# Kernel optimization log

Hardware: AMD Instinct MI355X
Metric: run time of the kernel (lower is better)

Reference implementation:

```python
import jax, jax.numpy as jnp
import numpy as np

B, S, D = 32, 2048, 64

def setup_inputs() -> dict:
    key = jax.random.key(0)
    kq, kk, kv = jax.random.split(key, 3)
    return {
        "query": jax.random.normal(kq, (B, S, D), dtype=jnp.float32),
        "key": jax.random.normal(kk, (B, S, D), dtype=jnp.float32),
        "value": jax.random.normal(kv, (B, S, D), dtype=jnp.float32),
    }

def reference(query, key, value):
    # scores: [B, S, S] = Q @ K^T / sqrt(d_k)  (scale=True)
    d_k = key.shape[-1]
    scores = jnp.einsum("bqd,bkd->bqk", query, key) / jnp.sqrt(jnp.asarray(d_k, query.dtype))
    # exp + normalize over last dim == softmax (no mask, dropout in eval mode)
    attn = jax.nn.softmax(scores, axis=-1)
    # context: [B, S, D] = attn @ V
    context = jnp.einsum("bqk,bkd->bqd", attn, value)
    return context
```

## Files before the change

### kernel.cpp

```cpp
#include <hip/hip_runtime.h>
#include <hip/hip_bf16.h>

#define B_   32
#define S_   2048
#define D_   64
#define KVB  64
#define NT   (S_/KVB)
#define NW   8
#define QW   32
#define QB   (NW*QW)

typedef __attribute__((ext_vector_type(8)))  __bf16 bf16x8;
typedef __attribute__((ext_vector_type(4)))  __bf16 bf16x4;
typedef __attribute__((ext_vector_type(16))) float  f32x16;

__device__ __forceinline__ float fexp2(float x) {
#if __has_builtin(__builtin_amdgcn_exp2f)
    return __builtin_amdgcn_exp2f(x);
#else
    return exp2f(x);
#endif
}

__device__ __forceinline__ unsigned pk2(float a, float b) {
    unsigned r;
    asm("v_cvt_pk_bf16_f32 %0, %1, %2" : "=v"(r) : "v"(a), "v"(b));
    return r;
}

__device__ __forceinline__ void pl32swap(unsigned &a, unsigned &b) {
#if __has_builtin(__builtin_amdgcn_permlane32_swap)
    auto r = __builtin_amdgcn_permlane32_swap(a, b, false, false);
    a = (unsigned)r[0]; b = (unsigned)r[1];
#else
    unsigned pa = (unsigned)__shfl_xor((int)a, 32);
    unsigned pb = (unsigned)__shfl_xor((int)b, 32);
    bool hi = (threadIdx.x & 32) != 0;
    unsigned na = hi ? pb : a;
    unsigned nb = hi ? b  : pa;
    a = na; b = nb;
#endif
}

__device__ __forceinline__ f32x16 z16() {
    f32x16 z;
    #pragma unroll
    for (int i = 0; i < 16; ++i) z[i] = 0.f;
    return z;
}

struct PBpair { bf16x8 a, b; };

__device__ __forceinline__ PBpair pack2(const f32x16 ps) {
    unsigned y0 = pk2(ps[0],  ps[1]);
    unsigned y1 = pk2(ps[2],  ps[3]);
    unsigned y2 = pk2(ps[4],  ps[5]);
    unsigned y3 = pk2(ps[6],  ps[7]);
    pl32swap(y0, y2); pl32swap(y1, y3);
    unsigned z0 = pk2(ps[8],  ps[9]);
    unsigned z1 = pk2(ps[10], ps[11]);
    unsigned z2 = pk2(ps[12], ps[13]);
    unsigned z3 = pk2(ps[14], ps[15]);
    pl32swap(z0, z2); pl32swap(z1, z3);
    union { unsigned u[4]; bf16x8 v; } pa, pbu;
    pa.u[0]=y0;  pa.u[1]=y1;  pa.u[2]=y2;  pa.u[3]=y3;
    pbu.u[0]=z0; pbu.u[1]=z1; pbu.u[2]=z2; pbu.u[3]=z3;
    PBpair r; r.a = pa.v; r.b = pbu.v; return r;
}

__global__ __launch_bounds__(512, 2)
void attn_fwd(const float* __restrict__ Q, const float* __restrict__ K,
              const float* __restrict__ V, float* __restrict__ Out)
{
    __shared__ __align__(16) __bf16 Kt[3][KVB * D_];
    __shared__ __align__(16) __bf16 Vt[3][D_ * KVB];

    const int tid  = threadIdx.x;
    const int w    = tid >> 6;
    const int lane = tid & 63;
    const int l31  = lane & 31;
    const int hi   = lane >> 5;

    const int bid = blockIdx.x;
    const int swz = ((bid & 7) << 5) | (bid >> 3);
    const int b   = swz >> 3;
    const int q0  = (swz & 7) * QB;

    const float SCL = 0.18033688011112042f;
    const float* qp = Q + ((size_t)(b*S_ + q0 + w*QW + l31))*D_ + hi*8;
    bf16x8 qf[4];
    #pragma unroll
    for (int ks = 0; ks < 4; ++ks) {
        float4 f0 = *reinterpret_cast<const float4*>(qp + ks*16);
        float4 f1 = *reinterpret_cast<const float4*>(qp + ks*16 + 4);
        bf16x8 a;
        a[0]=(__bf16)(f0.x*SCL); a[1]=(__bf16)(f0.y*SCL);
        a[2]=(__bf16)(f0.z*SCL); a[3]=(__bf16)(f0.w*SCL);
        a[4]=(__bf16)(f1.x*SCL); a[5]=(__bf16)(f1.y*SCL);
        a[6]=(__bf16)(f1.z*SCL); a[7]=(__bf16)(f1.w*SCL);
        qf[ks]=a;
    }

    int offK[4], offV[4];
    #pragma unroll
    for (int i = 0; i < 4; ++i) {
        offK[i] = l31*128 + (((i*32) + hi*16) ^ ((l31 & 7) << 4));
        offV[i] = l31*128 + (((i*32) + hi*16) ^ (((l31 >> 1) & 7) << 4));
    }

    const float* kg = K + (size_t)b*S_*D_;
    const float* vg = V + (size_t)b*S_*D_;

    const int krow0 = tid >> 4;
    const int kcol  = (tid & 15) * 4;
    const int kwr0  = krow0*128 + ((kcol*2) ^ ((krow0 & 7) << 4));
    const int kwr1  = kwr0 + 32*128;

    const int kv0 = (tid >> 4) * 2;
    const int db  = (tid & 15) * 2;
    int vwr[4];
    #pragma unroll
    for (int j = 0; j < 4; ++j) {
        int d = db + (j >> 1)*32 + (j & 1);
        vwr[j] = d*128 + ((kv0*2) ^ (((d >> 1) & 7) << 4));
    }

#define STAGE_LOAD(T)                                                              \
    {   const float* kt_ = kg + (size_t)(T)*KVB*D_;                                \
        const float* vt_ = vg + (size_t)(T)*KVB*D_;                                \
        ka  = *reinterpret_cast<const float4*>(kt_ + krow0*64 + kcol);             \
        kb  = *reinterpret_cast<const float4*>(kt_ + (krow0+32)*64 + kcol);        \
        va0 = *reinterpret_cast<const float2*>(vt_ + kv0*64 + db);                 \
        vb0 = *reinterpret_cast<const float2*>(vt_ + (kv0+1)*64 + db);             \
        va1 = *reinterpret_cast<const float2*>(vt_ + kv0*64 + db + 32);            \
        vb1 = *reinterpret_cast<const float2*>(vt_ + (kv0+1)*64 + db + 32);        }

#define STAGE_WRITE(BUF)                                                           \
    {   char* kw = (char*)&Kt[(BUF)][0];                                           \
        char* vw = (char*)&Vt[(BUF)][0];                                           \
        bf16x4 h0 = {(__bf16)ka.x,(__bf16)ka.y,(__bf16)ka.z,(__bf16)ka.w};         \
        bf16x4 h1 = {(__bf16)kb.x,(__bf16)kb.y,(__bf16)kb.z,(__bf16)kb.w};         \
        *reinterpret_cast<bf16x4*>(kw + kwr0) = h0;                                \
        *reinterpret_cast<bf16x4*>(kw + kwr1) = h1;                                \
        *reinterpret_cast<unsigned*>(vw + vwr[0]) = pk2(va0.x, vb0.x);             \
        *reinterpret_cast<unsigned*>(vw + vwr[1]) = pk2(va0.y, vb0.y);             \
        *reinterpret_cast<unsigned*>(vw + vwr[2]) = pk2(va1.x, vb1.x);             \
        *reinterpret_cast<unsigned*>(vw + vwr[3]) = pk2(va1.y, vb1.y);             }

    float4 ka, kb; float2 va0, vb0, va1, vb1;

    STAGE_LOAD(0)
    STAGE_WRITE(0)
    __syncthreads();

    float l_ = 0.f;
    f32x16 o0 = z16(), o1 = z16();
    PBpair p01, p23;

    {
        STAGE_LOAD(1)
        const char* kbuf = (const char*)&Kt[0][0];
        f32x16 s0 = z16(), s1 = z16();
        __builtin_amdgcn_s_setprio(1);
        #pragma unroll
        for (int ks = 0; ks < 4; ++ks) {
            bf16x8 k0 = *reinterpret_cast<const bf16x8*>(kbuf + offK[ks]);
            bf16x8 k1 = *reinterpret_cast<const bf16x8*>(kbuf + offK[ks] + 4096);
            s0 = __builtin_amdgcn_mfma_f32_32x32x16_bf16(k0, qf[ks], s0, 0,0,0);
            s1 = __builtin_amdgcn_mfma_f32_32x32x16_bf16(k1, qf[ks], s1, 0,0,0);
        }
        __builtin_amdgcn_s_setprio(0);
        #pragma unroll
        for (int r = 0; r < 16; ++r) s0[r] = fexp2(s0[r]);
        #pragma unroll
        for (int r = 0; r < 16; ++r) s1[r] = fexp2(s1[r]);
        float tsm[16];
        #pragma unroll
        for (int i = 0; i < 16; ++i) tsm[i] = s0[i] + s1[i];
        #pragma unroll
        for (int st = 8; st > 0; st >>= 1)
            #pragma unroll
            for (int i = 0; i < st; ++i) tsm[i] += tsm[i+st];
        l_ += tsm[0] + __shfl_xor(tsm[0], 32);
        p01 = pack2(s0);
        p23 = pack2(s1);
        STAGE_WRITE(1)
        __syncthreads();
    }

    for (int t = 1; t < NT; ++t) {
        const int cur = t % 3;
        const int prv = (t-1) % 3;
        const int nxt = (t+1) % 3;
        const int tn  = (t+1 < NT) ? (t+1) : t;
        STAGE_LOAD(tn)

        const char* kbuf = (const char*)&Kt[cur][0];
        const char* vbuf = (const char*)&Vt[prv][0];

        f32x16 s0 = z16(), s1 = z16();
        __builtin_amdgcn_s_setprio(1);
        #pragma unroll
        for (int ks = 0; ks < 4; ++ks) {
            bf16x8 k0 = *reinterpret_cast<const bf16x8*>(kbuf + offK[ks]);
            bf16x8 k1 = *reinterpret_cast<const bf16x8*>(kbuf + offK[ks] + 4096);
            s0 = __builtin_amdgcn_mfma_f32_32x32x16_bf16(k0, qf[ks], s0, 0,0,0);
            s1 = __builtin_amdgcn_mfma_f32_32x32x16_bf16(k1, qf[ks], s1, 0,0,0);
        }
        #define PV_STEP(c, pbf)                                                        \
        {   bf16x8 v0 = *reinterpret_cast<const bf16x8*>(vbuf + offV[c]);              \
            bf16x8 v1 = *reinterpret_cast<const bf16x8*>(vbuf + offV[c] + 4096);       \
            o0 = __builtin_amdgcn_mfma_f32_32x32x16_bf16(v0, pbf, o0, 0,0,0);          \
            o1 = __builtin_amdgcn_mfma_f32_32x32x16_bf16(v1, pbf, o1, 0,0,0);          }
        PV_STEP(0, p01.a)
        PV_STEP(1, p01.b)
        PV_STEP(2, p23.a)
        PV_STEP(3, p23.b)
        __builtin_amdgcn_s_setprio(0);

        #pragma unroll
        for (int r = 0; r < 16; ++r) s0[r] = fexp2(s0[r]);
        #pragma unroll
        for (int r = 0; r < 16; ++r) s1[r] = fexp2(s1[r]);
        float tsm[16];
        #pragma unroll
        for (int i = 0; i < 16; ++i) tsm[i] = s0[i] + s1[i];
        #pragma unroll
        for (int st = 8; st > 0; st >>= 1)
            #pragma unroll
            for (int i = 0; i < st; ++i) tsm[i] += tsm[i+st];
        l_ += tsm[0] + __shfl_xor(tsm[0], 32);
        p01 = pack2(s0);
        p23 = pack2(s1);

        STAGE_WRITE(nxt)
        __syncthreads();
    }

    {
        const char* vbuf = (const char*)&Vt[(NT-1) % 3][0];
        __builtin_amdgcn_s_setprio(1);
        PV_STEP(0, p01.a)
        PV_STEP(1, p01.b)
        PV_STEP(2, p23.a)
        PV_STEP(3, p23.b)
        __builtin_amdgcn_s_setprio(0);
        #undef PV_STEP
    }

    float invl = 1.0f / l_;
    float* orow = Out + ((size_t)(b*S_ + q0 + w*QW + l31))*D_;
    #pragma unroll
    for (int rr = 0; rr < 4; ++rr) {
        float4 res;
        res.x = o0[rr*4+0]*invl; res.y = o0[rr*4+1]*invl;
        res.z = o0[rr*4+2]*invl; res.w = o0[rr*4+3]*invl;
        *reinterpret_cast<float4*>(orow + rr*8 + hi*4) = res;
    }
    #pragma unroll
    for (int rr = 0; rr < 4; ++rr) {
        float4 res;
        res.x = o1[rr*4+0]*invl; res.y = o1[rr*4+1]*invl;
        res.z = o1[rr*4+2]*invl; res.w = o1[rr*4+3]*invl;
        *reinterpret_cast<float4*>(orow + 32 + rr*8 + hi*4) = res;
    }
}

extern "C" void kernel_launch(void* const* d_in, const int* in_sizes, int n_in,
                              void* d_out, int out_size, void* d_ws, size_t ws_size,
                              hipStream_t stream) {
    const float* Q = (const float*)d_in[0];
    const float* K = (const float*)d_in[1];
    const float* V = (const float*)d_in[2];
    float* O = (float*)d_out;
    attn_fwd<<<dim3(B_ * (S_ / QB)), dim3(512), 0, stream>>>(Q, K, V, O);
}
```

Before: 53.78 us.

## Process two KV half-tiles per stage to halve barriers and interleave softmax

Each loop iteration now loads and stages 128 KV rows as two 64-row halves, halving the number of stages and __syncthreads calls. Within a stage the QK of one half is interleaved with the PV of the previous half and the softmax of the other, keeping MFMA work overlapped with the exp and pack steps. Shared memory grows to 96 KB and registers rise because twice as many global loads are held in flight, and the occupancy hint of two blocks per CU is dropped, so fewer waves may be resident.

```diff
diff --git a/kernel.cpp b/kernel.cpp
--- a/kernel.cpp
+++ b/kernel.cpp
@@ -4,8 +4,7 @@
 #define B_   32
 #define S_   2048
 #define D_   64
-#define KVB  64
-#define NT   (S_/KVB)
+#define NT2  16
 #define NW   8
 #define QW   32
 #define QB   (NW*QW)
@@ -40,13 +39,6 @@
     unsigned nb = hi ? b  : pa;
     a = na; b = nb;
 #endif
-}
-
-__device__ __forceinline__ f32x16 z16() {
-    f32x16 z;
-    #pragma unroll
-    for (int i = 0; i < 16; ++i) z[i] = 0.f;
-    return z;
 }
 
 struct PBpair { bf16x8 a, b; };
@@ -68,12 +60,13 @@
     PBpair r; r.a = pa.v; r.b = pbu.v; return r;
 }
 
-__global__ __launch_bounds__(512, 2)
+__global__ __launch_bounds__(512)
 void attn_fwd(const float* __restrict__ Q, const float* __restrict__ K,
               const float* __restrict__ V, float* __restrict__ Out)
 {
-    __shared__ __align__(16) __bf16 Kt[3][KVB * D_];
-    __shared__ __align__(16) __bf16 Vt[3][D_ * KVB];
+    __shared__ __align__(16) char SMEM[3][2][2][8192];
+#define KT(BUF, H) (&SMEM[(BUF)][(H)][0][0])
+#define VT(BUF, H) (&SMEM[(BUF)][(H)][1][0])
 
     const int tid  = threadIdx.x;
     const int w    = tid >> 6;
@@ -87,18 +80,20 @@
     const int q0  = (swz & 7) * QB;
 
     const float SCL = 0.18033688011112042f;
-    const float* qp = Q + ((size_t)(b*S_ + q0 + w*QW + l31))*D_ + hi*8;
     bf16x8 qf[4];
-    #pragma unroll
-    for (int ks = 0; ks < 4; ++ks) {
-        float4 f0 = *reinterpret_cast<const float4*>(qp + ks*16);
-        float4 f1 = *reinterpret_cast<const float4*>(qp + ks*16 + 4);
-        bf16x8 a;
-        a[0]=(__bf16)(f0.x*SCL); a[1]=(__bf16)(f0.y*SCL);
-        a[2]=(__bf16)(f0.z*SCL); a[3]=(__bf16)(f0.w*SCL);
-        a[4]=(__bf16)(f1.x*SCL); a[5]=(__bf16)(f1.y*SCL);
-        a[6]=(__bf16)(f1.z*SCL); a[7]=(__bf16)(f1.w*SCL);
-        qf[ks]=a;
+    {
+        const float* qp = Q + ((size_t)(b*S_ + q0 + w*QW + l31))*D_ + hi*8;
+        #pragma unroll
+        for (int ks = 0; ks < 4; ++ks) {
+            float4 f0 = *reinterpret_cast<const float4*>(qp + ks*16);
+            float4 f1 = *reinterpret_cast<const float4*>(qp + ks*16 + 4);
+            bf16x8 a;
+            a[0]=(__bf16)(f0.x*SCL); a[1]=(__bf16)(f0.y*SCL);
+            a[2]=(__bf16)(f0.z*SCL); a[3]=(__bf16)(f0.w*SCL);
+            a[4]=(__bf16)(f1.x*SCL); a[5]=(__bf16)(f1.y*SCL);
+            a[6]=(__bf16)(f1.z*SCL); a[7]=(__bf16)(f1.w*SCL);
+            qf[ks]=a;
+        }
     }
 
     int offK[4], offV[4];
@@ -125,130 +120,122 @@
         vwr[j] = d*128 + ((kv0*2) ^ (((d >> 1) & 7) << 4));
     }
 
+    float4 ka[2][2];
+    float2 va0[2], vb0[2], va1[2], vb1[2];
+
 #define STAGE_LOAD(T)                                                              \
-    {   const float* kt_ = kg + (size_t)(T)*KVB*D_;                                \
-        const float* vt_ = vg + (size_t)(T)*KVB*D_;                                \
-        ka  = *reinterpret_cast<const float4*>(kt_ + krow0*64 + kcol);             \
-        kb  = *reinterpret_cast<const float4*>(kt_ + (krow0+32)*64 + kcol);        \
-        va0 = *reinterpret_cast<const float2*>(vt_ + kv0*64 + db);                 \
-        vb0 = *reinterpret_cast<const float2*>(vt_ + (kv0+1)*64 + db);             \
-        va1 = *reinterpret_cast<const float2*>(vt_ + kv0*64 + db + 32);            \
-        vb1 = *reinterpret_cast<const float2*>(vt_ + (kv0+1)*64 + db + 32);        }
+    {   _Pragma("unroll")                                                          \
+        for (int h = 0; h < 2; ++h) {                                              \
+            const float* kt_ = kg + ((size_t)(T)*128 + h*64)*64;                   \
+            const float* vt_ = vg + ((size_t)(T)*128 + h*64)*64;                   \
+            ka[h][0] = *reinterpret_cast<const float4*>(kt_ + krow0*64 + kcol);    \
+            ka[h][1] = *reinterpret_cast<const float4*>(kt_ + (krow0+32)*64 + kcol);\
+            va0[h] = *reinterpret_cast<const float2*>(vt_ + kv0*64 + db);          \
+            vb0[h] = *reinterpret_cast<const float2*>(vt_ + (kv0+1)*64 + db);      \
+            va1[h] = *reinterpret_cast<const float2*>(vt_ + kv0*64 + db + 32);     \
+            vb1[h] = *reinterpret_cast<const float2*>(vt_ + (kv0+1)*64 + db + 32); \
+        }                                                                          }
 
 #define STAGE_WRITE(BUF)                                                           \
-    {   char* kw = (char*)&Kt[(BUF)][0];                                           \
-        char* vw = (char*)&Vt[(BUF)][0];                                           \
-        bf16x4 h0 = {(__bf16)ka.x,(__bf16)ka.y,(__bf16)ka.z,(__bf16)ka.w};         \
-        bf16x4 h1 = {(__bf16)kb.x,(__bf16)kb.y,(__bf16)kb.z,(__bf16)kb.w};         \
-        *reinterpret_cast<bf16x4*>(kw + kwr0) = h0;                                \
-        *reinterpret_cast<bf16x4*>(kw + kwr1) = h1;                                \
-        *reinterpret_cast<unsigned*>(vw + vwr[0]) = pk2(va0.x, vb0.x);             \
-        *reinterpret_cast<unsigned*>(vw + vwr[1]) = pk2(va0.y, vb0.y);             \
-        *reinterpret_cast<unsigned*>(vw + vwr[2]) = pk2(va1.x, vb1.x);             \
-        *reinterpret_cast<unsigned*>(vw + vwr[3]) = pk2(va1.y, vb1.y);             }
-
-    float4 ka, kb; float2 va0, vb0, va1, vb1;
+    {   _Pragma("unroll")                                                          \
+        for (int h = 0; h < 2; ++h) {                                              \
+            char* kw = KT(BUF, h);                                                 \
+            char* vw = VT(BUF, h);                                                 \
+            bf16x4 h0 = {(__bf16)ka[h][0].x,(__bf16)ka[h][0].y,                    \
+                         (__bf16)ka[h][0].z,(__bf16)ka[h][0].w};                   \
+            bf16x4 h1 = {(__bf16)ka[h][1].x,(__bf16)ka[h][1].y,                    \
+                         (__bf16)ka[h][1].z,(__bf16)ka[h][1].w};                   \
+            *reinterpret_cast<bf16x4*>(kw + kwr0) = h0;                            \
+            *reinterpret_cast<bf16x4*>(kw + kwr1) = h1;                            \
+            *reinterpret_cast<unsigned*>(vw + vwr[0]) = pk2(va0[h].x, vb0[h].x);   \
+            *reinterpret_cast<unsigned*>(vw + vwr[1]) = pk2(va0[h].y, vb0[h].y);   \
+            *reinterpret_cast<unsigned*>(vw + vwr[2]) = pk2(va1[h].x, vb1[h].x);   \
+            *reinterpret_cast<unsigned*>(vw + vwr[3]) = pk2(va1[h].y, vb1[h].y);   \
+        }                                                                          }
+
+#define QK_H(BUF, H, s0, s1)                                                       \
+    {   const char* kbuf = (const char*)KT(BUF, H);                                \
+        __builtin_amdgcn_s_setprio(1);                                             \
+        _Pragma("unroll")                                                          \
+        for (int ks = 0; ks < 4; ++ks) {                                           \
+            bf16x8 k0 = *reinterpret_cast<const bf16x8*>(kbuf + offK[ks]);         \
+            bf16x8 k1 = *reinterpret_cast<const bf16x8*>(kbuf + offK[ks] + 4096);  \
+            s0 = __builtin_amdgcn_mfma_f32_32x32x16_bf16(k0, qf[ks], s0, 0,0,0);   \
+            s1 = __builtin_amdgcn_mfma_f32_32x32x16_bf16(k1, qf[ks], s1, 0,0,0);   \
+        }                                                                          \
+        __builtin_amdgcn_s_setprio(0);                                             }
+
+#define PV_H(BUF, H, P01, P23)                                                     \
+    {   const char* vbuf = (const char*)VT(BUF, H);                                \
+        __builtin_amdgcn_s_setprio(1);                                             \
+        _Pragma("unroll")                                                          \
+        for (int c = 0; c < 4; ++c) {                                              \
+            bf16x8 pf = (c==0)?P01.a:(c==1)?P01.b:(c==2)?P23.a:P23.b;              \
+            bf16x8 v0 = *reinterpret_cast<const bf16x8*>(vbuf + offV[c]);          \
+            bf16x8 v1 = *reinterpret_cast<const bf16x8*>(vbuf + offV[c] + 4096);   \
+            o0 = __builtin_amdgcn_mfma_f32_32x32x16_bf16(v0, pf, o0, 0,0,0);       \
+            o1 = __builtin_amdgcn_mfma_f32_32x32x16_bf16(v1, pf, o1, 0,0,0);       \
+        }                                                                          \
+        __builtin_amdgcn_s_setprio(0);                                             }
+
+#define SM_PACK(s0, s1, P01, P23)                                                  \
+    {   _Pragma("unroll")                                                          \
+        for (int r = 0; r < 16; ++r) s0[r] = fexp2(s0[r]);                         \
+        _Pragma("unroll")                                                          \
+        for (int r = 0; r < 16; ++r) s1[r] = fexp2(s1[r]);                         \
+        float tsm[16];                                                             \
+        _Pragma("unroll")                                                          \
+        for (int i = 0; i < 16; ++i) tsm[i] = s0[i] + s1[i];                       \
+        _Pragma("unroll")                                                          \
+        for (int st = 8; st > 0; st >>= 1)                                         \
+            _Pragma("unroll")                                                      \
+            for (int i = 0; i < st; ++i) tsm[i] += tsm[i+st];                      \
+        l_ += tsm[0] + __shfl_xor(tsm[0], 32);                                     \
+        P01 = pack2(s0); P23 = pack2(s1);                                          }
+
+    float l_ = 0.f;
+    f32x16 o0, o1;
+    #pragma unroll
+    for (int i = 0; i < 16; ++i) { o0[i] = 0.f; o1[i] = 0.f; }
+
+    PBpair pc01, pc23;
 
     STAGE_LOAD(0)
     STAGE_WRITE(0)
     __syncthreads();
 
-    float l_ = 0.f;
-    f32x16 o0 = z16(), o1 = z16();
-    PBpair p01, p23;
-
-    {
-        STAGE_LOAD(1)
-        const char* kbuf = (const char*)&Kt[0][0];
-        f32x16 s0 = z16(), s1 = z16();
-        __builtin_amdgcn_s_setprio(1);
+    for (int t = 0; t < NT2; ++t) {
+        const int cur = t % 3;
+        const int prv = (t + 2) % 3;
+        const int nxt = (t + 1) % 3;
+        STAGE_LOAD(t+1 < NT2 ? t+1 : t)
+
+        f32x16 s0, s1;
         #pragma unroll
-        for (int ks = 0; ks < 4; ++ks) {
-            bf16x8 k0 = *reinterpret_cast<const bf16x8*>(kbuf + offK[ks]);
-            bf16x8 k1 = *reinterpret_cast<const bf16x8*>(kbuf + offK[ks] + 4096);
-            s0 = __builtin_amdgcn_mfma_f32_32x32x16_bf16(k0, qf[ks], s0, 0,0,0);
-            s1 = __builtin_amdgcn_mfma_f32_32x32x16_bf16(k1, qf[ks], s1, 0,0,0);
-        }
-        __builtin_amdgcn_s_setprio(0);
+        for (int i = 0; i < 16; ++i) { s0[i] = 0.f; s1[i] = 0.f; }
+        QK_H(cur, 0, s0, s1)
+
+        if (t > 0) { PV_H(prv, 1, pc01, pc23) }
+
+        PBpair pa01, pa23;
+        SM_PACK(s0, s1, pa01, pa23)
+
+        f32x16 u0, u1;
         #pragma unroll
-        for (int r = 0; r < 16; ++r) s0[r] = fexp2(s0[r]);
-        #pragma unroll
-        for (int r = 0; r < 16; ++r) s1[r] = fexp2(s1[r]);
-        float tsm[16];
-        #pragma unroll
-        for (int i = 0; i < 16; ++i) tsm[i] = s0[i] + s1[i];
-        #pragma unroll
-        for (int st = 8; st > 0; st >>= 1)
-            #pragma unroll
-            for (int i = 0; i < st; ++i) tsm[i] += tsm[i+st];
-        l_ += tsm[0] + __shfl_xor(tsm[0], 32);
-        p01 = pack2(s0);
-        p23 = pack2(s1);
-        STAGE_WRITE(1)
+        for (int i = 0; i < 16; ++i) { u0[i] = 0.f; u1[i] = 0.f; }
+        QK_H(cur, 1, u0, u1)
+
+        PV_H(cur, 0, pa01, pa23)
+
+        SM_PACK(u0, u1, pc01, pc23)
+
+        if (t+1 < NT2) STAGE_WRITE(nxt)
         __syncthreads();
     }
 
-    for (int t = 1; t < NT; ++t) {
-        const int cur = t % 3;
-        const int prv = (t-1) % 3;
-        const int nxt = (t+1) % 3;
-        const int tn  = (t+1 < NT) ? (t+1) : t;
-        STAGE_LOAD(tn)
-
-        const char* kbuf = (const char*)&Kt[cur][0];
-        const char* vbuf = (const char*)&Vt[prv][0];
-
-        f32x16 s0 = z16(), s1 = z16();
-        __builtin_amdgcn_s_setprio(1);
-        #pragma unroll
-        for (int ks = 0; ks < 4; ++ks) {
-            bf16x8 k0 = *reinterpret_cast<const bf16x8*>(kbuf + offK[ks]);
-            bf16x8 k1 = *reinterpret_cast<const bf16x8*>(kbuf + offK[ks] + 4096);
-            s0 = __builtin_amdgcn_mfma_f32_32x32x16_bf16(k0, qf[ks], s0, 0,0,0);
-            s1 = __builtin_amdgcn_mfma_f32_32x32x16_bf16(k1, qf[ks], s1, 0,0,0);
-        }
-        #define PV_STEP(c, pbf)                                                        \
-        {   bf16x8 v0 = *reinterpret_cast<const bf16x8*>(vbuf + offV[c]);              \
-            bf16x8 v1 = *reinterpret_cast<const bf16x8*>(vbuf + offV[c] + 4096);       \
-            o0 = __builtin_amdgcn_mfma_f32_32x32x16_bf16(v0, pbf, o0, 0,0,0);          \
-            o1 = __builtin_amdgcn_mfma_f32_32x32x16_bf16(v1, pbf, o1, 0,0,0);          }
-        PV_STEP(0, p01.a)
-        PV_STEP(1, p01.b)
-        PV_STEP(2, p23.a)
-        PV_STEP(3, p23.b)
-        __builtin_amdgcn_s_setprio(0);
-
-        #pragma unroll
-        for (int r = 0; r < 16; ++r) s0[r] = fexp2(s0[r]);
-        #pragma unroll
-        for (int r = 0; r < 16; ++r) s1[r] = fexp2(s1[r]);
-        float tsm[16];
-        #pragma unroll
-        for (int i = 0; i < 16; ++i) tsm[i] = s0[i] + s1[i];
-        #pragma unroll
-        for (int st = 8; st > 0; st >>= 1)
-            #pragma unroll
-            for (int i = 0; i < st; ++i) tsm[i] += tsm[i+st];
-        l_ += tsm[0] + __shfl_xor(tsm[0], 32);
-        p01 = pack2(s0);
-        p23 = pack2(s1);
-
-        STAGE_WRITE(nxt)
-        __syncthreads();
-    }
-
-    {
-        const char* vbuf = (const char*)&Vt[(NT-1) % 3][0];
-        __builtin_amdgcn_s_setprio(1);
-        PV_STEP(0, p01.a)
-        PV_STEP(1, p01.b)
-        PV_STEP(2, p23.a)
-        PV_STEP(3, p23.b)
-        __builtin_amdgcn_s_setprio(0);
-        #undef PV_STEP
-    }
-
-    float invl = 1.0f / l_;
+    PV_H((NT2-1) % 3, 1, pc01, pc23)
+
+    const float invl = 1.0f / l_;
     float* orow = Out + ((size_t)(b*S_ + q0 + w*QW + l31))*D_;
     #pragma unroll
     for (int rr = 0; rr < 4; ++rr) {
```

Result: faster. 51.61 us (-4.0%).
